# Optimization experiments

Measured on AMD Instinct MI355X. Metric: run time of the kernel, lower is better.

The kernel has to match this reference:

```python
import jax, jax.numpy as jnp
import numpy as np


def setup_inputs() -> dict:
    key = jax.random.key(0)
    k1, k2 = jax.random.split(key)
    B, P, N, M = 8, 32, 1024, 1024
    normalized_receptive_fields = jax.random.normal(k1, (B, P, N, 3), dtype=jnp.float32)
    reconstructed_points = jax.random.normal(k2, (B, P, M, 3), dtype=jnp.float32)
    return {
        "normalized_receptive_fields": normalized_receptive_fields,
        "reconstructed_points": reconstructed_points,
    }


def reference(normalized_receptive_fields, reconstructed_points):
    B, P, M, _ = reconstructed_points.shape
    N = normalized_receptive_fields.shape[2]
    # Faithful to torch: permute(0,1,3,2) then reshape(-1, M, 3).
    x = jnp.transpose(reconstructed_points, (0, 1, 3, 2)).reshape(-1, M, 3)  # (BP, M, 3)
    y = normalized_receptive_fields.reshape(-1, N, 3)                        # (BP, N, 3)
    xx = jnp.sum(x * x, axis=-1)                 # (BP, M)
    yy = jnp.sum(y * y, axis=-1)                 # (BP, N)
    xy = jnp.einsum('bmc,bnc->bmn', x, y)        # (BP, M, N)
    dist = xx[:, :, None] + yy[:, None, :] - 2.0 * xy  # (BP, M, N)
    min_x_to_y = jnp.min(dist, axis=2)           # (BP, M)
    min_y_to_x = jnp.min(dist, axis=1)           # (BP, N)
    return jnp.mean(min_x_to_y) + jnp.mean(min_y_to_x)
```

## Files before the change

kernel.cpp:

```cpp
#include <hip/hip_runtime.h>


#define MM 1024
#define NN 1024
#define THREADS 1024
#define NWAVES 16
#define FINF 3.4e38f

typedef float f32x16 __attribute__((ext_vector_type(16)));
typedef __bf16 bf16x8 __attribute__((ext_vector_type(8)));

#define B_STRIDE 80
#define A_STRIDE 64
#define B_OFF 0
#define A_OFF (NN * B_STRIDE)
#define CW_OFF A_OFF
#define RS_OFF (A_OFF + MM * A_STRIDE)
#define RED_OFF (RS_OFF + 128)
#define LDS_BYTES (RED_OFF + 64)

__device__ __forceinline__ unsigned short bf16_rne(float v) {
    unsigned u = __float_as_uint(v);
    u = u + 0x7FFFu + ((u >> 16) & 1u);
    return (unsigned short)(u >> 16);
}
__device__ __forceinline__ float bf16f(unsigned short h) {
    return __uint_as_float(((unsigned)h) << 16);
}
struct S3 { unsigned short h0, h1, h2; };
__device__ __forceinline__ S3 split3(float v) {
    S3 o;
    o.h0 = bf16_rne(v);
    float r = v - bf16f(o.h0);
    o.h1 = bf16_rne(r);
    float r2 = r - bf16f(o.h1);
    o.h2 = bf16_rne(r2);
    return o;
}
__device__ __forceinline__ unsigned pk(unsigned short a, unsigned short b) {
    return (unsigned)a | ((unsigned)b << 16);
}
__device__ __forceinline__ float min3f(float a, float b, float c) {
    return fminf(fminf(a, b), c);
}
template <int CTRL>
__device__ __forceinline__ float dpp_ror_min(float v) {
    int vi = __float_as_int(v);
    int t  = __builtin_amdgcn_update_dpp(vi, vi, CTRL, 0xf, 0xf, true);
    return fminf(v, __int_as_float(t));
}

__global__ __launch_bounds__(THREADS, 4)
void chamfer_kernel(const float* __restrict__ nrf,
                    const float* __restrict__ rp,
                    float* __restrict__ out,
                    float inv_bpm, float inv_bpn) {
    __shared__ __align__(16) unsigned char smem[LDS_BYTES];
    unsigned char* Bb = smem + B_OFF;
    unsigned short* As = (unsigned short*)(smem + A_OFF);
    float* colW = (float*)(smem + CW_OFF);
    float* rowsumS = (float*)(smem + RS_OFF);
    float* redS = (float*)(smem + RED_OFF);

    const int bp = blockIdx.x;
    const int tid = threadIdx.x;
    const int lane = tid & 63;
    const int wave = tid >> 6;
    const int l31 = lane & 31;
    const int lh = lane >> 5;
    const unsigned short ONE = 0x3F80;

    const float* yB = nrf + (size_t)bp * NN * 3;
    const float* xB = rp + (size_t)bp * MM * 3;

    {
        const int c = tid;
        float y0 = yB[c * 3 + 0], y1 = yB[c * 3 + 1], y2 = yB[c * 3 + 2];
        float yy = __builtin_fmaf(y0, y0, __builtin_fmaf(y1, y1, y2 * y2));
        S3 b0 = split3(y0), b1 = split3(y1), b2 = split3(y2), q = split3(yy);
        uint4* dst = (uint4*)(Bb + c * B_STRIDE);
        dst[0] = make_uint4(pk(b0.h0, b0.h1), pk(b0.h0, b0.h1), pk(b0.h2, b0.h0), pk(b1.h0, b1.h1));
        dst[1] = make_uint4(pk(b1.h0, b1.h1), pk(b1.h2, b1.h0), pk(b2.h0, b2.h1), pk(b2.h0, b2.h1));
        dst[2] = make_uint4(pk(b2.h2, b2.h0), pk(ONE, ONE), pk(ONE, q.h0), pk(q.h1, q.h2));
        dst[3] = make_uint4(pk(b0.h2, b0.h1), pk(b1.h2, b1.h1), pk(b2.h2, b2.h1), 0u);
        dst[4] = make_uint4(0u, 0u, 0u, 0u);
    }
    {
        const int m = tid;
        int k = 3 * m;
        float x0 = xB[((k    ) & (MM - 1)) * 3 + ((k    ) >> 10)];
        float x1 = xB[((k + 1) & (MM - 1)) * 3 + ((k + 1) >> 10)];
        float x2 = xB[((k + 2) & (MM - 1)) * 3 + ((k + 2) >> 10)];
        float xx = __builtin_fmaf(x0, x0, __builtin_fmaf(x1, x1, x2 * x2));
        S3 a0 = split3(-2.0f * x0), a1 = split3(-2.0f * x1), a2 = split3(-2.0f * x2);
        S3 p = split3(xx);
        uint4* dst = (uint4*)((unsigned char*)As + m * A_STRIDE);
        dst[0] = make_uint4(pk(a0.h0, a0.h0), pk(a0.h1, a0.h1), pk(a0.h0, a0.h2), pk(a1.h0, a1.h0));
        dst[1] = make_uint4(pk(a1.h1, a1.h1), pk(a1.h0, a1.h2), pk(a2.h0, a2.h0), pk(a2.h1, a2.h1));
        dst[2] = make_uint4(pk(a2.h0, a2.h2), pk(p.h0, p.h1), pk(p.h2, ONE), pk(ONE, ONE));
        dst[3] = make_uint4(pk(a0.h1, a0.h2), pk(a1.h1, a1.h2), pk(a2.h1, a2.h2), 0u);
    }
    __syncthreads();

    const int m0 = wave * 64;
    bf16x8 af[2][2];
    #pragma unroll
    for (int s = 0; s < 2; ++s) {
        #pragma unroll
        for (int h = 0; h < 2; ++h)
            af[s][h] = *(const bf16x8*)(As + (m0 + s * 32 + l31) * 32 + h * 16 + lh * 8);
    }
    __syncthreads();

    float rmin[2][16];
    #pragma unroll
    for (int s = 0; s < 2; ++s)
        #pragma unroll
        for (int j = 0; j < 16; ++j) rmin[s][j] = FINF;

    f32x16 Z = {};
    const unsigned char* bptr = Bb + l31 * B_STRIDE + lh * 16;
    const int xaddr32 = (lane ^ 32) << 2;
    float* colWrow = colW + wave * 1024;

    bf16x8 bf0 = *(const bf16x8*)(bptr);
    bf16x8 bf1 = *(const bf16x8*)(bptr + 32);
    for (int t = 0; t < 32; ++t) {
        const unsigned char* np = bptr + 32 * B_STRIDE;
        bf16x8 nb0 = *(const bf16x8*)(np);
        bf16x8 nb1 = *(const bf16x8*)(np + 32);

        float cm = FINF;
        #pragma unroll
        for (int s = 0; s < 2; ++s) {
            f32x16 acc = __builtin_amdgcn_mfma_f32_32x32x16_bf16(af[s][0], bf0, Z, 0, 0, 0);
            acc = __builtin_amdgcn_mfma_f32_32x32x16_bf16(af[s][1], bf1, acc, 0, 0, 0);
            #pragma unroll
            for (int j = 0; j < 16; ++j) rmin[s][j] = fminf(rmin[s][j], acc[j]);
            float u0 = min3f(acc[0], acc[1], acc[2]);
            float u1 = min3f(acc[3], acc[4], acc[5]);
            float u2 = min3f(acc[6], acc[7], acc[8]);
            float u3 = min3f(acc[9], acc[10], acc[11]);
            float u4 = min3f(acc[12], acc[13], acc[14]);
            cm = fminf(cm, fminf(min3f(u0, u1, u2), min3f(u3, u4, acc[15])));
        }
        int pz = __builtin_amdgcn_ds_bpermute(xaddr32, __float_as_int(cm));
        cm = fminf(cm, __int_as_float(pz));
        if (lh == 0) colWrow[t * 32 + l31] = cm;

        bf0 = nb0; bf1 = nb1; bptr = np;
    }

    float rowsum = 0.0f;
    #pragma unroll
    for (int s = 0; s < 2; ++s) {
        #pragma unroll
        for (int j = 0; j < 16; ++j) {
            float v = rmin[s][j];
            v = dpp_ror_min<0x121>(v);
            v = dpp_ror_min<0x122>(v);
            v = dpp_ror_min<0x124>(v);
            v = dpp_ror_min<0x128>(v);
            int sw = __builtin_amdgcn_ds_swizzle(__float_as_int(v), 0x401F);
            v = fminf(v, __int_as_float(sw));
            rowsum += v;
        }
    }
    if (l31 == 0) rowsumS[wave * 2 + lh] = rowsum;
    __syncthreads();

    {
        const int c = tid;
        float v = colW[c];
        #pragma unroll
        for (int w = 1; w < NWAVES; ++w) v = fminf(v, colW[w * 1024 + c]);
        float csum = v;
        #pragma unroll
        for (int off = 32; off > 0; off >>= 1) csum += __shfl_xor(csum, off, 64);
        if (lane == 0) redS[wave] = csum;
    }
    __syncthreads();

    if (tid == 0) {
        float rs = 0.0f, cs = 0.0f;
        #pragma unroll
        for (int w = 0; w < NWAVES; ++w) cs += redS[w];
        #pragma unroll
        for (int w = 0; w < 2 * NWAVES; ++w) rs += rowsumS[w];
        atomicAdd(out, rs * inv_bpm + cs * inv_bpn);
    }
}

extern "C" void kernel_launch(void* const* d_in, const int* in_sizes, int n_in,
                              void* d_out, int out_size, void* d_ws, size_t ws_size,
                              hipStream_t stream) {
    const float* nrf = (const float*)d_in[0];
    const float* rp  = (const float*)d_in[1];
    float* out = (float*)d_out;

    const int BP = in_sizes[1] / (MM * 3);
    const float inv_bpm = 1.0f / (float)(BP * MM);
    const float inv_bpn = 1.0f / (float)(BP * NN);

    (void)hipMemsetAsync(out, 0, sizeof(float), stream);
    chamfer_kernel<<<BP, THREADS, 0, stream>>>(nrf, rp, out, inv_bpm, inv_bpn);
}
```

Measured before the change: 99.41 us.

## Split each batch over two blocks with 16x16 MFMA and LDS atomic column mins

Each (b,p) problem is now split across two blocks, each handling half of the M rows, which doubles the grid size. The kernel switches to 16x16x32 bf16 MFMA with fragments built directly in registers. Per-tile column minima are combined with LDS atomicMin on order-preserving integer keys instead of per-wave column buffers. A second small kernel merges the two halves' column minima through workspace memory. This is meant to raise occupancy and parallelism, at the cost of an extra launch, global round-trips and LDS atomic contention.

```diff
diff --git a/kernel.cpp b/kernel.cpp
--- a/kernel.cpp
+++ b/kernel.cpp
@@ -7,17 +7,13 @@
 #define NWAVES 16
 #define FINF 3.4e38f
 
-typedef float f32x16 __attribute__((ext_vector_type(16)));
+typedef float f32x4 __attribute__((ext_vector_type(4)));
 typedef __bf16 bf16x8 __attribute__((ext_vector_type(8)));
 
-#define B_STRIDE 80
-#define A_STRIDE 64
-#define B_OFF 0
-#define A_OFF (NN * B_STRIDE)
-#define CW_OFF A_OFF
-#define RS_OFF (A_OFF + MM * A_STRIDE)
-#define RED_OFF (RS_OFF + 128)
-#define LDS_BYTES (RED_OFF + 64)
+#define BT_OFF 0
+#define CK_OFF 65536
+#define RS_OFF (CK_OFF + 8192)
+#define LDS_BYTES (RS_OFF + 64)
 
 __device__ __forceinline__ unsigned short bf16_rne(float v) {
     unsigned u = __float_as_uint(v);
@@ -49,25 +45,31 @@
     int t  = __builtin_amdgcn_update_dpp(vi, vi, CTRL, 0xf, 0xf, true);
     return fminf(v, __int_as_float(t));
 }
-
-__global__ __launch_bounds__(THREADS, 4)
-void chamfer_kernel(const float* __restrict__ nrf,
-                    const float* __restrict__ rp,
-                    float* __restrict__ out,
-                    float inv_bpm, float inv_bpn) {
+__device__ __forceinline__ unsigned fkey(float v) {
+    unsigned u = __float_as_uint(v);
+    return ((int)u < 0) ? ~u : (u | 0x80000000u);
+}
+__device__ __forceinline__ float unkey(unsigned k) {
+    return ((int)k < 0) ? __uint_as_float(k & 0x7FFFFFFFu) : __uint_as_float(~k);
+}
+
+__global__ __launch_bounds__(THREADS, 8)
+void chamfer_main(const float* __restrict__ nrf,
+                  const float* __restrict__ rp,
+                  float* __restrict__ colP,
+                  float* __restrict__ out,
+                  float inv_bpm) {
     __shared__ __align__(16) unsigned char smem[LDS_BYTES];
-    unsigned char* Bb = smem + B_OFF;
-    unsigned short* As = (unsigned short*)(smem + A_OFF);
-    float* colW = (float*)(smem + CW_OFF);
+    unsigned* colK = (unsigned*)(smem + CK_OFF);
     float* rowsumS = (float*)(smem + RS_OFF);
-    float* redS = (float*)(smem + RED_OFF);
-
-    const int bp = blockIdx.x;
-    const int tid = threadIdx.x;
+
+    const int bp   = blockIdx.x >> 1;
+    const int half = blockIdx.x & 1;
+    const int tid  = threadIdx.x;
     const int lane = tid & 63;
     const int wave = tid >> 6;
-    const int l31 = lane & 31;
-    const int lh = lane >> 5;
+    const int l15  = lane & 15;
+    const int g    = lane >> 4;
     const unsigned short ONE = 0x3F80;
 
     const float* yB = nrf + (size_t)bp * NN * 3;
@@ -78,116 +80,118 @@
         float y0 = yB[c * 3 + 0], y1 = yB[c * 3 + 1], y2 = yB[c * 3 + 2];
         float yy = __builtin_fmaf(y0, y0, __builtin_fmaf(y1, y1, y2 * y2));
         S3 b0 = split3(y0), b1 = split3(y1), b2 = split3(y2), q = split3(yy);
-        uint4* dst = (uint4*)(Bb + c * B_STRIDE);
+        uint4* dst = (uint4*)(smem + BT_OFF + (c >> 4) * 1024 + (c & 15) * 64);
         dst[0] = make_uint4(pk(b0.h0, b0.h1), pk(b0.h0, b0.h1), pk(b0.h2, b0.h0), pk(b1.h0, b1.h1));
         dst[1] = make_uint4(pk(b1.h0, b1.h1), pk(b1.h2, b1.h0), pk(b2.h0, b2.h1), pk(b2.h0, b2.h1));
         dst[2] = make_uint4(pk(b2.h2, b2.h0), pk(ONE, ONE), pk(ONE, q.h0), pk(q.h1, q.h2));
         dst[3] = make_uint4(pk(b0.h2, b0.h1), pk(b1.h2, b1.h1), pk(b2.h2, b2.h1), 0u);
-        dst[4] = make_uint4(0u, 0u, 0u, 0u);
-    }
-    {
-        const int m = tid;
-        int k = 3 * m;
+        colK[c] = 0xFFFFFFFFu;
+        colK[1024 + c] = 0xFFFFFFFFu;
+    }
+
+    bf16x8 af[2];
+    #pragma unroll
+    for (int s = 0; s < 2; ++s) {
+        const int m = half * 512 + wave * 32 + s * 16 + l15;
+        const int k = 3 * m;
         float x0 = xB[((k    ) & (MM - 1)) * 3 + ((k    ) >> 10)];
         float x1 = xB[((k + 1) & (MM - 1)) * 3 + ((k + 1) >> 10)];
         float x2 = xB[((k + 2) & (MM - 1)) * 3 + ((k + 2) >> 10)];
         float xx = __builtin_fmaf(x0, x0, __builtin_fmaf(x1, x1, x2 * x2));
         S3 a0 = split3(-2.0f * x0), a1 = split3(-2.0f * x1), a2 = split3(-2.0f * x2);
         S3 p = split3(xx);
-        uint4* dst = (uint4*)((unsigned char*)As + m * A_STRIDE);
-        dst[0] = make_uint4(pk(a0.h0, a0.h0), pk(a0.h1, a0.h1), pk(a0.h0, a0.h2), pk(a1.h0, a1.h0));
-        dst[1] = make_uint4(pk(a1.h1, a1.h1), pk(a1.h0, a1.h2), pk(a2.h0, a2.h0), pk(a2.h1, a2.h1));
-        dst[2] = make_uint4(pk(a2.h0, a2.h2), pk(p.h0, p.h1), pk(p.h2, ONE), pk(ONE, ONE));
-        dst[3] = make_uint4(pk(a0.h1, a0.h2), pk(a1.h1, a1.h2), pk(a2.h1, a2.h2), 0u);
+        uint4 q0 = make_uint4(pk(a0.h0, a0.h0), pk(a0.h1, a0.h1), pk(a0.h0, a0.h2), pk(a1.h0, a1.h0));
+        uint4 q1 = make_uint4(pk(a1.h1, a1.h1), pk(a1.h0, a1.h2), pk(a2.h0, a2.h0), pk(a2.h1, a2.h1));
+        uint4 q2 = make_uint4(pk(a2.h0, a2.h2), pk(p.h0, p.h1), pk(p.h2, ONE), pk(ONE, ONE));
+        uint4 q3 = make_uint4(pk(a0.h1, a0.h2), pk(a1.h1, a1.h2), pk(a2.h1, a2.h2), 0u);
+        uint4 sel = (g == 0) ? q0 : (g == 1) ? q1 : (g == 2) ? q2 : q3;
+        union { uint4 u; bf16x8 b; } cv; cv.u = sel;
+        af[s] = cv.b;
     }
     __syncthreads();
 
-    const int m0 = wave * 64;
-    bf16x8 af[2][2];
+    const unsigned fragoff = (unsigned)((l15 * 4 + g) * 16);
+    const unsigned char* BtBase = smem + BT_OFF;
+    unsigned* colKme = colK + (lane >> 5) * 1024 + l15;
+    const f32x4 Z = {0.0f, 0.0f, 0.0f, 0.0f};
+
+    float rmin0[4], rmin1[4];
+    #pragma unroll
+    for (int j = 0; j < 4; ++j) { rmin0[j] = FINF; rmin1[j] = FINF; }
+
+    bf16x8 bfc = *(const bf16x8*)(BtBase + fragoff);
+    #pragma unroll
+    for (int t = 0; t < 64; ++t) {
+        bf16x8 bfn = *(const bf16x8*)(BtBase + (t + 1) * 1024 + fragoff);
+
+        f32x4 acc0 = __builtin_amdgcn_mfma_f32_16x16x32_bf16(af[0], bfc, Z, 0, 0, 0);
+        f32x4 acc1 = __builtin_amdgcn_mfma_f32_16x16x32_bf16(af[1], bfc, Z, 0, 0, 0);
+
+        #pragma unroll
+        for (int j = 0; j < 4; ++j) rmin0[j] = fminf(rmin0[j], acc0[j]);
+        #pragma unroll
+        for (int j = 0; j < 4; ++j) rmin1[j] = fminf(rmin1[j], acc1[j]);
+
+        float cm0 = fminf(min3f(acc0[0], acc0[1], acc0[2]), acc0[3]);
+        float cm1 = fminf(min3f(acc1[0], acc1[1], acc1[2]), acc1[3]);
+        float cm = fminf(cm0, cm1);
+        int sw = __builtin_amdgcn_ds_swizzle(__float_as_int(cm), 0x401F);
+        cm = fminf(cm, __int_as_float(sw));
+        atomicMin(colKme + t * 16, fkey(cm));
+
+        bfc = bfn;
+    }
+
+    float rowsum = 0.0f;
     #pragma unroll
     for (int s = 0; s < 2; ++s) {
         #pragma unroll
-        for (int h = 0; h < 2; ++h)
-            af[s][h] = *(const bf16x8*)(As + (m0 + s * 32 + l31) * 32 + h * 16 + lh * 8);
-    }
-    __syncthreads();
-
-    float rmin[2][16];
-    #pragma unroll
-    for (int s = 0; s < 2; ++s)
-        #pragma unroll
-        for (int j = 0; j < 16; ++j) rmin[s][j] = FINF;
-
-    f32x16 Z = {};
-    const unsigned char* bptr = Bb + l31 * B_STRIDE + lh * 16;
-    const int xaddr32 = (lane ^ 32) << 2;
-    float* colWrow = colW + wave * 1024;
-
-    bf16x8 bf0 = *(const bf16x8*)(bptr);
-    bf16x8 bf1 = *(const bf16x8*)(bptr + 32);
-    for (int t = 0; t < 32; ++t) {
-        const unsigned char* np = bptr + 32 * B_STRIDE;
-        bf16x8 nb0 = *(const bf16x8*)(np);
-        bf16x8 nb1 = *(const bf16x8*)(np + 32);
-
-        float cm = FINF;
-        #pragma unroll
-        for (int s = 0; s < 2; ++s) {
-            f32x16 acc = __builtin_amdgcn_mfma_f32_32x32x16_bf16(af[s][0], bf0, Z, 0, 0, 0);
-            acc = __builtin_amdgcn_mfma_f32_32x32x16_bf16(af[s][1], bf1, acc, 0, 0, 0);
-            #pragma unroll
-            for (int j = 0; j < 16; ++j) rmin[s][j] = fminf(rmin[s][j], acc[j]);
-            float u0 = min3f(acc[0], acc[1], acc[2]);
-            float u1 = min3f(acc[3], acc[4], acc[5]);
-            float u2 = min3f(acc[6], acc[7], acc[8]);
-            float u3 = min3f(acc[9], acc[10], acc[11]);
-            float u4 = min3f(acc[12], acc[13], acc[14]);
-            cm = fminf(cm, fminf(min3f(u0, u1, u2), min3f(u3, u4, acc[15])));
-        }
-        int pz = __builtin_amdgcn_ds_bpermute(xaddr32, __float_as_int(cm));
-        cm = fminf(cm, __int_as_float(pz));
-        if (lh == 0) colWrow[t * 32 + l31] = cm;
-
-        bf0 = nb0; bf1 = nb1; bptr = np;
-    }
-
-    float rowsum = 0.0f;
-    #pragma unroll
-    for (int s = 0; s < 2; ++s) {
-        #pragma unroll
-        for (int j = 0; j < 16; ++j) {
-            float v = rmin[s][j];
+        for (int j = 0; j < 4; ++j) {
+            float v = (s == 0) ? rmin0[j] : rmin1[j];
             v = dpp_ror_min<0x121>(v);
             v = dpp_ror_min<0x122>(v);
             v = dpp_ror_min<0x124>(v);
             v = dpp_ror_min<0x128>(v);
-            int sw = __builtin_amdgcn_ds_swizzle(__float_as_int(v), 0x401F);
-            v = fminf(v, __int_as_float(sw));
             rowsum += v;
         }
     }
-    if (l31 == 0) rowsumS[wave * 2 + lh] = rowsum;
+    rowsum += __int_as_float(__builtin_amdgcn_ds_swizzle(__float_as_int(rowsum), 0x401F));
+    rowsum += __int_as_float(__builtin_amdgcn_ds_bpermute((lane ^ 32) << 2, __float_as_int(rowsum)));
+    if (lane == 0) rowsumS[wave] = rowsum;
     __syncthreads();
 
     {
-        const int c = tid;
-        float v = colW[c];
-        #pragma unroll
-        for (int w = 1; w < NWAVES; ++w) v = fminf(v, colW[w * 1024 + c]);
-        float csum = v;
-        #pragma unroll
-        for (int off = 32; off > 0; off >>= 1) csum += __shfl_xor(csum, off, 64);
-        if (lane == 0) redS[wave] = csum;
-    }
+        unsigned k0 = colK[tid], k1 = colK[1024 + tid];
+        colP[(size_t)blockIdx.x * 1024 + tid] = unkey(k0 < k1 ? k0 : k1);
+    }
+    if (tid < 64) {
+        float r = (tid < 16) ? rowsumS[tid] : 0.0f;
+        #pragma unroll
+        for (int off = 8; off > 0; off >>= 1) r += __shfl_xor(r, off, 64);
+        if (tid == 0) atomicAdd(out, r * inv_bpm);
+    }
+}
+
+__global__ __launch_bounds__(1024)
+void chamfer_reduce(const float* __restrict__ colP, float* __restrict__ out,
+                    float inv_bpn) {
+    const int bp = blockIdx.x;
+    const int tid = threadIdx.x;
+    const int lane = tid & 63;
+    const int wave = tid >> 6;
+    __shared__ float ws[16];
+
+    float v = fminf(colP[(size_t)(2 * bp) * 1024 + tid],
+                    colP[(size_t)(2 * bp + 1) * 1024 + tid]);
+    #pragma unroll
+    for (int off = 32; off > 0; off >>= 1) v += __shfl_xor(v, off, 64);
+    if (lane == 0) ws[wave] = v;
     __syncthreads();
-
     if (tid == 0) {
-        float rs = 0.0f, cs = 0.0f;
-        #pragma unroll
-        for (int w = 0; w < NWAVES; ++w) cs += redS[w];
-        #pragma unroll
-        for (int w = 0; w < 2 * NWAVES; ++w) rs += rowsumS[w];
-        atomicAdd(out, rs * inv_bpm + cs * inv_bpn);
+        float s = 0.0f;
+        #pragma unroll
+        for (int w = 0; w < 16; ++w) s += ws[w];
+        atomicAdd(out, s * inv_bpn);
     }
 }
 
@@ -197,11 +201,13 @@
     const float* nrf = (const float*)d_in[0];
     const float* rp  = (const float*)d_in[1];
     float* out = (float*)d_out;
+    float* colP = (float*)d_ws;
 
     const int BP = in_sizes[1] / (MM * 3);
     const float inv_bpm = 1.0f / (float)(BP * MM);
     const float inv_bpn = 1.0f / (float)(BP * NN);
 
     (void)hipMemsetAsync(out, 0, sizeof(float), stream);
-    chamfer_kernel<<<BP, THREADS, 0, stream>>>(nrf, rp, out, inv_bpm, inv_bpn);
-}
+    chamfer_main<<<BP * 2, THREADS, 0, stream>>>(nrf, rp, colP, out, inv_bpm);
+    chamfer_reduce<<<BP, 1024, 0, stream>>>(colP, out, inv_bpn);
+}
```

Result: faster. 89.45 us (-10.0%).
